# Kernel optimization log

Hardware: AMD Instinct MI355X
Metric: run time of the kernel (lower is better)

## Reference

```python
import jax, jax.numpy as jnp
import numpy as np

TOPK = 5

def _l2norm(x, axis):
    n = jnp.sqrt(jnp.sum(x * x, axis=axis, keepdims=True))
    return x / jnp.maximum(n, 1e-12)

def _conv_block(x, w, b, g, beta):
    # Conv2d(k=3, stride=2, pad=1) + BatchNorm (train-mode batch stats) + ReLU + AvgPool2d(3,1,pad=1)
    x = jax.lax.conv_general_dilated(x, w, (2, 2), ((1, 1), (1, 1)),
                                     dimension_numbers=('NCHW', 'OIHW', 'NCHW'))
    x = x + b[None, :, None, None]
    mean = jnp.mean(x, axis=(0, 2, 3), keepdims=True)
    var = jnp.mean((x - mean) ** 2, axis=(0, 2, 3), keepdims=True)
    x = (x - mean) * jax.lax.rsqrt(var + 1e-5) * g[None, :, None, None] + beta[None, :, None, None]
    x = jax.nn.relu(x)
    # AvgPool2d default count_include_pad=True -> always divide by 9
    x = jax.lax.reduce_window(x, 0.0, jax.lax.add, (1, 1, 3, 3), (1, 1, 1, 1),
                              ((0, 0), (0, 0), (1, 1), (1, 1))) / 9.0
    return x

def _encode(x, params):
    x = x[:, None]  # B,1,T,D
    for (w, b, g, beta) in params:
        x = _conv_block(x, w, b, g, beta)
    return jnp.mean(x, axis=(2, 3))  # AdaptiveAvgPool2d(1) + flatten

def setup_inputs() -> dict:
    key = jax.random.key(0)
    ks = jax.random.split(key, 8)
    B, T, D = 128, 1024, 128
    dim, capQ, refD = 128, 2048, 2304
    inp = {}
    inp['feats'] = jax.random.normal(ks[0], (B, 2, T, D), jnp.float32)
    inp['ref_feats'] = jax.random.normal(ks[1], (B, refD), jnp.float32)
    inp['indices'] = jax.random.randint(ks[2], (B,), 0, 10000)
    mq = jax.random.normal(ks[3], (dim, capQ), jnp.float32)
    inp['MoCoQueue'] = mq / jnp.maximum(jnp.linalg.norm(mq, axis=0, keepdims=True), 1e-12)
    rq = jax.random.normal(ks[4], (refD, capQ), jnp.float32)
    inp['RefQueue'] = rq / jnp.maximum(jnp.linalg.norm(rq, axis=0, keepdims=True), 1e-12)
    inp['IndexQueue'] = jax.random.randint(ks[5], (capQ,), 0, 10000).astype(jnp.float32)
    chans = [1, 4, 16, 64, 128]
    pk = jax.random.split(ks[6], 4)
    for i in range(4):
        ci, co = chans[i], chans[i + 1]
        inp['w%d' % (i + 1)] = jax.random.normal(pk[i], (co, ci, 3, 3), jnp.float32) * 0.1
        inp['b%d' % (i + 1)] = jnp.zeros((co,), jnp.float32)
        inp['g%d' % (i + 1)] = jnp.ones((co,), jnp.float32)
        inp['be%d' % (i + 1)] = jnp.zeros((co,), jnp.float32)
    return inp

def reference(feats, ref_feats, indices, MoCoQueue, RefQueue, IndexQueue,
              w1, b1, g1, be1, w2, b2, g2, be2, w3, b3, g3, be3, w4, b4, g4, be4):
    params = [(w1, b1, g1, be1), (w2, b2, g2, be2), (w3, b3, g3, be3), (w4, b4, g4, be4)]
    q = _l2norm(_encode(feats[:, 1], params), 1)                      # B,dim
    k = jax.lax.stop_gradient(_l2norm(_encode(feats[:, 0], params), 1))
    ref = _l2norm(ref_feats, 1)                                       # B,2304
    B = q.shape[0]
    score_pos = jnp.sum(q * k, axis=1, keepdims=True)                 # B,1
    score_neg = q @ jax.lax.stop_gradient(MoCoQueue)                  # B,capQ
    mask = indices[:, None].astype(IndexQueue.dtype) == IndexQueue[None, :]  # B,capQ bool
    # queue_full=True branch: topk over reference queue similarities + scatter reweighting
    score_ref = ref @ jax.lax.stop_gradient(RefQueue)                 # B,capQ
    masked = jnp.where(mask, -jnp.inf, score_ref)
    _, idx = jax.lax.top_k(masked, TOPK)                              # B,topK
    score_ref2 = jnp.where(mask, 1.0, score_ref)
    rows = jnp.arange(B)[:, None]
    weighted = jnp.full_like(score_neg, -1.0).at[rows, idx].set(1.0)
    mask_f = mask.astype(jnp.float32).at[rows, idx].set(1.0)
    score_neg = score_neg * score_ref2 * weighted
    score = jnp.concatenate([score_pos, score_neg], axis=1)           # B,1+capQ
    mask_out = jnp.concatenate([jnp.ones((B, 1), jnp.float32), mask_f], axis=1)
    return score, mask_out
```

## Files before the change

### kernel.cpp

```cpp
#include <hip/hip_runtime.h>


#define NIMG 128
typedef __attribute__((ext_vector_type(8))) short bf16x8;
typedef __attribute__((ext_vector_type(4))) float f32x4;
typedef __attribute__((ext_vector_type(4))) unsigned int u32x4;
typedef unsigned long long ull;

__device__ __forceinline__ unsigned short f2bf(float f) {
  unsigned u = __float_as_uint(f);
  unsigned r = (u + 0x7fffu + ((u >> 16) & 1u)) >> 16;
  return (unsigned short)r;
}
__device__ __forceinline__ float bf2f(unsigned short u) {
  return __uint_as_float((unsigned)u << 16);
}

__global__ __launch_bounds__(256) void wtr4_k(
    const float* __restrict__ w2, const float* __restrict__ w3,
    const float* __restrict__ w4, unsigned short* __restrict__ wb2,
    unsigned short* __restrict__ wb3, unsigned short* __restrict__ wb4) {
  const int i = blockIdx.x * 256 + threadIdx.x;
  if (i < 16 * 64) {
    int co = i / 64, k = i % 64;
    int tap = k >> 2, ci = k & 3;
    float v = (k < 36) ? w2[co * 36 + ci * 9 + tap] : 0.f;
    wb2[i] = f2bf(v);
  }
  if (i < 64 * 160) {
    int co = i / 160, k = i % 160;
    int tap = k >> 4, ci = k & 15;
    float v = (k < 144) ? w3[co * 144 + ci * 9 + tap] : 0.f;
    wb3[i] = f2bf(v);
  }
  if (i < 128 * 576) {
    int co = i / 576, k = i % 576;
    int tap = k / 64, ci = k & 63;
    wb4[i] = f2bf(w4[co * 576 + ci * 9 + tap]);
  }
}

__device__ __forceinline__ void l1row(const float* __restrict__ ib, int ih,
                                      int w0i, float* r) {
  if (ih < 0) {
#pragma unroll
    for (int q = 0; q < 9; ++q) r[q] = 0.f;
    return;
  }
  const float* rp = ib + ih * 128 + 2 * w0i;
  const float4 a = *(const float4*)rp;
  const float4 b = *(const float4*)(rp + 4);
  r[0] = (w0i > 0) ? rp[-1] : 0.f;
  r[1] = a.x; r[2] = a.y; r[3] = a.z; r[4] = a.w;
  r[5] = b.x; r[6] = b.y; r[7] = b.z; r[8] = b.w;
}

__global__ __launch_bounds__(256, 4) void conv1s_k(const float* __restrict__ feats,
    const float* __restrict__ w1, const float* __restrict__ b1,
    unsigned short* __restrict__ y, float* __restrict__ part1,
    float* __restrict__ part2) {
  constexpr int TH = 4;
  const int tid = threadIdx.x;
  const int lw = tid & 15, grp = tid >> 4;
  const int h0 = (blockIdx.x * 16 + grp) * TH;
  const int pn = blockIdx.z;
  const int p = pn >> 7, n = pn & 127;
  const int sel = (p == 0) ? 1 : 0;
  const float* ib = feats + (size_t)(n * 2 + sel) * 131072;
  const int w0i = lw * 4;

  float wgt[36];
#pragma unroll
  for (int t = 0; t < 36; ++t) wgt[t] = w1[t];
  float bv[4];
#pragma unroll
  for (int c = 0; c < 4; ++c) bv[c] = b1[c];

  float r[9][9];
#pragma unroll
  for (int j = 0; j < 9; ++j) l1row(ib, 2 * h0 - 1 + j, w0i, r[j]);

  float s1[4] = {0.f, 0.f, 0.f, 0.f}, s2[4] = {0.f, 0.f, 0.f, 0.f};
#pragma unroll
  for (int t = 0; t < TH; ++t) {
    const int h = h0 + t;
    const float* r0 = r[2 * t];
    const float* r1 = r[2 * t + 1];
    const float* r2 = r[2 * t + 2];
#pragma unroll
    for (int co = 0; co < 4; ++co) {
      unsigned short ob[4];
#pragma unroll
      for (int i = 0; i < 4; ++i) {
        float v = bv[co];
#pragma unroll
        for (int kw = 0; kw < 3; ++kw) {
          v = fmaf(wgt[co * 9 + kw],     r0[2 * i + kw], v);
          v = fmaf(wgt[co * 9 + 3 + kw], r1[2 * i + kw], v);
          v = fmaf(wgt[co * 9 + 6 + kw], r2[2 * i + kw], v);
        }
        ob[i] = f2bf(v);
        s1[co] += v; s2[co] += v * v;
      }
      const ull o = (ull)ob[0] | ((ull)ob[1] << 16) | ((ull)ob[2] << 32)
                  | ((ull)ob[3] << 48);
      *(ull*)(y + (((size_t)pn * 4 + co) * 512 + h) * 64 + w0i) = o;
    }
  }
  __shared__ float ws1[4][4], ws2[4][4];
  const int lane = tid & 63, wid = tid >> 6;
#pragma unroll
  for (int co = 0; co < 4; ++co) {
#pragma unroll
    for (int m = 32; m >= 1; m >>= 1) {
      s1[co] += __shfl_xor(s1[co], m);
      s2[co] += __shfl_xor(s2[co], m);
    }
    if (lane == 0) { ws1[wid][co] = s1[co]; ws2[wid][co] = s2[co]; }
  }
  __syncthreads();
  if (tid < 4) {
    const float t1 = ws1[0][tid] + ws1[1][tid] + ws1[2][tid] + ws1[3][tid];
    const float t2 = ws2[0][tid] + ws2[1][tid] + ws2[2][tid] + ws2[3][tid];
    const int nblk = gridDim.x * 128;
    const int blk = (pn & 127) * gridDim.x + blockIdx.x;
    part1[(size_t)(p * 4 + tid) * nblk + blk] = t1;
    part2[(size_t)(p * 4 + tid) * nblk + blk] = t2;
  }
}

template<int Cin, int H, int W, int M, int SPB, int KP, int KC, int WCO, int WSP,
         int Cout, int MSPLIT>
__global__ __launch_bounds__(256) void cgemmi_k(
    const unsigned short* __restrict__ x,
    const unsigned short* __restrict__ wb,
    const float* __restrict__ bias, unsigned short* __restrict__ y,
    float* __restrict__ part1, float* __restrict__ part2) {
  constexpr int Ho = H / 2, Wo = W / 2, HWout = Ho * Wo;
  constexpr int lgWo = (Wo == 8 ? 3 : (Wo == 16 ? 4 : 5));
  constexpr int lgCin = (Cin == 4 ? 2 : (Cin == 16 ? 4 : 6));
  constexpr int MB = M / MSPLIT;
  constexpr int KCP = KC + 8;
  constexpr int MT = WCO / 16, NT = WSP / 16, KS = KC / 32;
  constexpr int NWN = SPB / WSP;
  constexpr int GR = (Cin < 8) ? 4 : 8;
  __shared__ unsigned short wl[MB][KCP];
  __shared__ unsigned short bl[SPB][KCP];
  __shared__ float ss1[MB], ss2[MB];
  const int tid = threadIdx.x;
  const int pnl = blockIdx.y;
  const int p = pnl >> 7;
  const int spc = blockIdx.x / MSPLIT;
  const int mc = blockIdx.x - spc * MSPLIT;
  const int sp0 = spc * SPB;
  const int m0 = mc * MB;
  const int lane = tid & 63, wid = tid >> 6;
  const int wm = wid / NWN, wn = wid - wm * NWN;
  const int l15 = lane & 15, lg = lane >> 4;
  const unsigned short* xb = x + (size_t)pnl * Cin * (H * W);

  for (int i = tid; i < MB; i += 256) { ss1[i] = 0.f; ss2[i] = 0.f; }

  f32x4 acc[MT][NT];
#pragma unroll
  for (int mt = 0; mt < MT; ++mt)
#pragma unroll
    for (int nt = 0; nt < NT; ++nt) acc[mt][nt] = (f32x4){0.f, 0.f, 0.f, 0.f};

  for (int k0 = 0; k0 < KP; k0 += KC) {
    for (int it = tid; it < MB * (KC / 8); it += 256) {
      const int row = it / (KC / 8), seg = it - row * (KC / 8);
      const u32x4 v = *(const u32x4*)(wb + (size_t)(m0 + row) * KP + k0 + seg * 8);
      *(u32x4*)(&wl[row][seg * 8]) = v;
    }
    for (int it = tid; it < SPB * (KC / GR); it += 256) {
      const int row = it / (KC / GR);
      const int rem = it - row * (KC / GR);
      const int k = k0 + rem * GR;
      const int tap = k >> lgCin;
      const int ci0 = k & (Cin - 1);
      const int sp = sp0 + row;
      const int ho = sp >> lgWo, wo = sp & (Wo - 1);
      const int kh = tap / 3, kw = tap - kh * 3;
      const int ih = 2 * ho - 1 + kh, iw = 2 * wo - 1 + kw;
      unsigned short* dst = &bl[row][k - k0];
      if (tap < 9 && (unsigned)ih < (unsigned)H && (unsigned)iw < (unsigned)W) {
        const unsigned short* src = xb + ((size_t)(ih * W + iw) * Cin + ci0);
        if constexpr (GR == 4) {
          *(ull*)dst = *(const ull*)src;
        } else {
          *(u32x4*)dst = *(const u32x4*)src;
        }
      } else {
        *(ull*)dst = 0ull;
        if constexpr (GR == 8) *(ull*)(dst + 4) = 0ull;
      }
    }
    __syncthreads();
#pragma unroll
    for (int ks = 0; ks < KS; ++ks) {
      bf16x8 af[MT], bfr[NT];
#pragma unroll
      for (int mt = 0; mt < MT; ++mt)
        af[mt] = *(const bf16x8*)(&wl[wm * WCO + mt * 16 + l15][ks * 32 + lg * 8]);
#pragma unroll
      for (int nt = 0; nt < NT; ++nt)
        bfr[nt] = *(const bf16x8*)(&bl[wn * WSP + nt * 16 + l15][ks * 32 + lg * 8]);
#pragma unroll
      for (int mt = 0; mt < MT; ++mt)
#pragma unroll
        for (int nt = 0; nt < NT; ++nt)
          acc[mt][nt] = __builtin_amdgcn_mfma_f32_16x16x32_bf16(af[mt], bfr[nt], acc[mt][nt], 0, 0, 0);
    }
    __syncthreads();
  }

  unsigned short* yb = y + (size_t)pnl * Cout * HWout;
#pragma unroll
  for (int mt = 0; mt < MT; ++mt) {
#pragma unroll
    for (int i = 0; i < 4; ++i) {
      const int col = wm * WCO + mt * 16 + lg * 4 + i;
      const int co = m0 + col;
      const float bv = bias[co];
      float s1 = 0.f, s2 = 0.f;
#pragma unroll
      for (int nt = 0; nt < NT; ++nt) {
        const float v = acc[mt][nt][i] + bv;
        yb[(size_t)co * HWout + sp0 + wn * WSP + nt * 16 + l15] = f2bf(v);
        s1 += v; s2 += v * v;
      }
#pragma unroll
      for (int m = 1; m < 16; m <<= 1) { s1 += __shfl_xor(s1, m); s2 += __shfl_xor(s2, m); }
      if (l15 == 0) {
        atomicAdd(&ss1[col], s1);
        atomicAdd(&ss2[col], s2);
      }
    }
  }
  __syncthreads();
  const int nspc = gridDim.x / MSPLIT;
  const int nblk = nspc * 128;
  const int blkid = (pnl & 127) * nspc + spc;
  for (int i = tid; i < MB; i += 256) {
    part1[(size_t)(p * Cout + m0 + i) * nblk + blkid] = ss1[i];
    part2[(size_t)(p * Cout + m0 + i) * nblk + blkid] = ss2[i];
  }
}

__global__ __launch_bounds__(256) void redstat_k(const float* __restrict__ p1,
    const float* __restrict__ p2, float* __restrict__ st, int nblk) {
  const int row = blockIdx.x;
  float s1 = 0.f, s2 = 0.f;
  for (int i = threadIdx.x; i < nblk; i += 256) {
    s1 += p1[(size_t)row * nblk + i];
    s2 += p2[(size_t)row * nblk + i];
  }
  __shared__ float r1[256], r2[256];
  r1[threadIdx.x] = s1; r2[threadIdx.x] = s2;
  __syncthreads();
  for (int stp = 128; stp > 0; stp >>= 1) {
    if (threadIdx.x < stp) {
      r1[threadIdx.x] += r1[threadIdx.x + stp];
      r2[threadIdx.x] += r2[threadIdx.x + stp];
    }
    __syncthreads();
  }
  if (threadIdx.x == 0) {
    st[row] = r1[0];
    st[256 + row] = r2[0];
  }
}

template<int W>
__device__ __forceinline__ void row_hs(const unsigned short* __restrict__ yp,
                                       int hh, int H, int w0, float a, float b,
                                       float* hs) {
  if ((unsigned)hh >= (unsigned)H) { hs[0] = hs[1] = hs[2] = hs[3] = 0.f; return; }
  const unsigned short* rp = yp + hh * W;
  const ull B = *(const ull*)(rp + w0);
  float r0 = 0.f, r5 = 0.f;
  if (w0 > 0) r0 = fmaxf(fmaf(a, bf2f(rp[w0 - 1]), b), 0.f);
  if (w0 + 4 < W) r5 = fmaxf(fmaf(a, bf2f(rp[w0 + 4]), b), 0.f);
  const float r1 = fmaxf(fmaf(a, bf2f((unsigned short)(B & 0xffff)), b), 0.f);
  const float r2 = fmaxf(fmaf(a, bf2f((unsigned short)((B >> 16) & 0xffff)), b), 0.f);
  const float r3 = fmaxf(fmaf(a, bf2f((unsigned short)((B >> 32) & 0xffff)), b), 0.f);
  const float r4 = fmaxf(fmaf(a, bf2f((unsigned short)(B >> 48)), b), 0.f);
  hs[0] = r0 + r1 + r2;
  hs[1] = r1 + r2 + r3;
  hs[2] = r2 + r3 + r4;
  hs[3] = r3 + r4 + r5;
}

template<int Cout, int H, int W>
__global__ __launch_bounds__(256) void bnpool7_k(const unsigned short* __restrict__ y,
    const float* __restrict__ st, const float* __restrict__ g,
    const float* __restrict__ be, unsigned short* __restrict__ x4, float invCnt) {
  constexpr int W4 = W / 4;
  constexpr int lgW4 = (W4 == 16 ? 4 : (W4 == 8 ? 3 : 2));
  constexpr int NCG = Cout / 4;
  constexpr int lgNCG = (NCG == 1 ? 0 : (NCG == 4 ? 2 : 4));
  constexpr int HQ = 256 >> (lgW4 + lgNCG);
  constexpr int TH = 4;
  constexpr int R = HQ * TH;
  constexpr int RS = W * Cout;
  constexpr int RSP = RS + 8;
  constexpr int HW = H * W;
  __shared__ unsigned short lbuf[R * RSP];
  const int tid = threadIdx.x;
  const int wq = tid & (W4 - 1);
  const int cg = (tid >> lgW4) & (NCG - 1);
  const int hq = tid >> (lgW4 + lgNCG);
  const int w0 = wq * 4;
  const int c0 = cg * 4;
  const int h0 = blockIdx.x * R;
  const int ht0 = h0 + hq * TH;
  const int pn = blockIdx.z;
  const int p = pn >> 7;

  float a[4], b[4];
#pragma unroll
  for (int j = 0; j < 4; ++j) {
    const int c = c0 + j;
    const float mean = st[p * Cout + c] * invCnt;
    const float var = fmaxf(st[256 + p * Cout + c] * invCnt - mean * mean, 0.f);
    a[j] = g[c] * rsqrtf(var + 1e-5f);
    b[j] = be[c] - mean * a[j];
  }
  const unsigned short* yb = y + (size_t)pn * Cout * (size_t)HW;

  float hsA[4][4], hsB[4][4], hsC[4][4];
#pragma unroll
  for (int j = 0; j < 4; ++j)
    row_hs<W>(yb + (size_t)(c0 + j) * HW, ht0 - 1, H, w0, a[j], b[j], hsA[j]);
#pragma unroll
  for (int j = 0; j < 4; ++j)
    row_hs<W>(yb + (size_t)(c0 + j) * HW, ht0, H, w0, a[j], b[j], hsB[j]);
#pragma unroll
  for (int t = 0; t < TH; ++t) {
    const int h = ht0 + t;
    const int lh = hq * TH + t;
#pragma unroll
    for (int j = 0; j < 4; ++j)
      row_hs<W>(yb + (size_t)(c0 + j) * HW, h + 1, H, w0, a[j], b[j], hsC[j]);
#pragma unroll
    for (int i = 0; i < 4; ++i) {
      unsigned short ob[4];
#pragma unroll
      for (int j = 0; j < 4; ++j)
        ob[j] = f2bf((hsA[j][i] + hsB[j][i] + hsC[j][i]) * (1.f / 9.f));
      const ull o = (ull)ob[0] | ((ull)ob[1] << 16) | ((ull)ob[2] << 32)
                  | ((ull)ob[3] << 48);
      *(ull*)(&lbuf[lh * RSP + (w0 + i) * Cout + c0]) = o;
    }
#pragma unroll
    for (int j = 0; j < 4; ++j)
#pragma unroll
      for (int i = 0; i < 4; ++i) { hsA[j][i] = hsB[j][i]; hsB[j][i] = hsC[j][i]; }
  }
  __syncthreads();
  unsigned short* xp = x4 + ((size_t)pn * HW + (size_t)h0 * W) * Cout;
  constexpr int SEGS = RS / 8;
  for (int it = tid; it < R * SEGS; it += 256) {
    const int row = it / SEGS, seg = it - row * SEGS;
    const u32x4 v = *(const u32x4*)(&lbuf[row * RSP + seg * 8]);
    *(u32x4*)(xp + (size_t)row * RS + seg * 8) = v;
  }
}

template<int Cout, int H, int W, int TH>
__global__ __launch_bounds__(256) void bnpool3_k(const unsigned short* __restrict__ y,
    const float* __restrict__ st, const float* __restrict__ g,
    const float* __restrict__ be, unsigned short* __restrict__ x, float invCnt) {
  constexpr int W4 = W / 4;
  constexpr int GROUPS = 256 / W4;
  constexpr int HW = H * W;
  const int tid = threadIdx.x;
  const int grp = tid / W4, lw = tid - grp * W4;
  const int w0 = lw * 4;
  const int h0 = (blockIdx.x * GROUPS + grp) * TH;
  if (h0 >= H) return;
  const int pn = blockIdx.z, c = blockIdx.y;
  const int p = pn >> 7;
  const float mean = st[p * Cout + c] * invCnt;
  const float var = fmaxf(st[256 + p * Cout + c] * invCnt - mean * mean, 0.f);
  const float a = g[c] * rsqrtf(var + 1e-5f);
  const float b = be[c] - mean * a;
  const unsigned short* yp = y + ((size_t)pn * Cout + c) * (size_t)HW;
  unsigned short* xp = x + ((size_t)pn * Cout + c) * (size_t)HW;

  float hsA[4], hsB[4], hsC[4];
  row_hs<W>(yp, h0 - 1, H, w0, a, b, hsA);
  row_hs<W>(yp, h0, H, w0, a, b, hsB);
#pragma unroll
  for (int t = 0; t < TH; ++t) {
    const int h = h0 + t;
    if (h >= H) break;
    row_hs<W>(yp, h + 1, H, w0, a, b, hsC);
    const ull o = (ull)f2bf((hsA[0] + hsB[0] + hsC[0]) * (1.f / 9.f))
                | ((ull)f2bf((hsA[1] + hsB[1] + hsC[1]) * (1.f / 9.f)) << 16)
                | ((ull)f2bf((hsA[2] + hsB[2] + hsC[2]) * (1.f / 9.f)) << 32)
                | ((ull)f2bf((hsA[3] + hsB[3] + hsC[3]) * (1.f / 9.f)) << 48);
    *(ull*)(xp + h * W + w0) = o;
#pragma unroll
    for (int i = 0; i < 4; ++i) { hsA[i] = hsB[i]; hsB[i] = hsC[i]; }
  }
}

__global__ __launch_bounds__(256) void feat2_k(const unsigned short* __restrict__ x,
    float* __restrict__ qk, float* __restrict__ qkT) {
  const int pn = blockIdx.x;
  const int tid = threadIdx.x;
  const int lane = tid & 63, wid = tid >> 6;
  __shared__ float fm[128];
  __shared__ float red[128];
  const unsigned short* xb = x + (size_t)pn * 128 * 512;
  for (int c = wid; c < 128; c += 4) {
    const unsigned short* xp = xb + (size_t)c * 512;
    float s = 0.f;
#pragma unroll
    for (int r = 0; r < 4; ++r) {
      const unsigned v = *(const unsigned*)(xp + lane * 2 + r * 128);
      s += bf2f((unsigned short)(v & 0xffff)) + bf2f((unsigned short)(v >> 16));
    }
#pragma unroll
    for (int m = 32; m >= 1; m >>= 1) s += __shfl_xor(s, m);
    if (lane == 0) fm[c] = s * (1.f / 512.f);
  }
  __syncthreads();
  if (tid < 128) red[tid] = fm[tid] * fm[tid];
  __syncthreads();
  for (int step = 64; step > 0; step >>= 1) {
    if (tid < step) red[tid] += red[tid + step];
    __syncthreads();
  }
  const float inv = 1.f / fmaxf(sqrtf(red[0]), 1e-12f);
  if (tid < 128) {
    const float v = fm[tid] * inv;
    qk[(size_t)pn * 128 + tid] = v;
    if (pn < 128) qkT[(size_t)tid * 128 + pn] = v;
  }
}

__global__ __launch_bounds__(256) void refnorm_k(const float* __restrict__ rf,
    float* __restrict__ rinv) {
  const int n = blockIdx.x;
  float s = 0.f;
  for (int i = threadIdx.x; i < 2304; i += 256) {
    float v = rf[(size_t)n * 2304 + i];
    s += v * v;
  }
  __shared__ float red[256];
  red[threadIdx.x] = s;
  __syncthreads();
  for (int step = 128; step > 0; step >>= 1) {
    if (threadIdx.x < step) red[threadIdx.x] += red[threadIdx.x + step];
    __syncthreads();
  }
  if (threadIdx.x == 0) rinv[n] = 1.f / fmaxf(sqrtf(red[0]), 1e-12f);
}

__global__ __launch_bounds__(256) void reft_k(const float* __restrict__ rf,
    const float* __restrict__ rinv, float* __restrict__ rfT) {
  const int flat = blockIdx.x * 256 + threadIdx.x;
  const int n = flat / 2304, k = flat - n * 2304;
  rfT[(size_t)k * 128 + n] = rf[flat] * rinv[n];
}

__global__ __launch_bounds__(256) void sneg2_k(const float* __restrict__ qkT,
    const float* __restrict__ moco, float* __restrict__ out) {
  const int j = blockIdx.x * 256 + threadIdx.x;
  const int n0 = blockIdx.y * 8;
  float acc[8] = {0.f};
#pragma unroll 4
  for (int k = 0; k < 128; ++k) {
    const float rv = moco[(size_t)k * 2048 + j];
    const float* qp = qkT + (size_t)k * 128 + n0;
#pragma unroll
    for (int i = 0; i < 8; ++i) acc[i] = fmaf(qp[i], rv, acc[i]);
  }
#pragma unroll
  for (int i = 0; i < 8; ++i) out[(size_t)(n0 + i) * 2048 + j] = acc[i];
}

template<int KCH>
__global__ __launch_bounds__(256) void sref3_k(const float* __restrict__ rfT,
    const float* __restrict__ rq, float* __restrict__ part) {
  const int j = blockIdx.x * 256 + threadIdx.x;
  const int n0 = blockIdx.y * 8;
  const int kc = blockIdx.z;
  const int kbeg = kc * KCH;
  float acc[8] = {0.f};
#pragma unroll 4
  for (int k = kbeg; k < kbeg + KCH; ++k) {
    const float rv = rq[(size_t)k * 2048 + j];
    const float* rp = rfT + (size_t)k * 128 + n0;
#pragma unroll
    for (int i = 0; i < 8; ++i) acc[i] = fmaf(rp[i], rv, acc[i]);
  }
  float* pb = part + (size_t)kc * (128 * 2048);
#pragma unroll
  for (int i = 0; i < 8; ++i) pb[(size_t)(n0 + i) * 2048 + j] = acc[i];
}

template<int NCH>
__global__ __launch_bounds__(256) void sredr_k(const float* __restrict__ part,
    float* __restrict__ out) {
  const int j = blockIdx.x * 256 + threadIdx.x;
  const int n = blockIdx.y;
  const size_t off = (size_t)n * 2048 + j;
  float s = 0.f;
#pragma unroll
  for (int c = 0; c < NCH; ++c) s += part[(size_t)c * (128 * 2048) + off];
  out[off] = s;
}

__global__ __launch_bounds__(256) void topk_k(const float* __restrict__ sref,
    const float* __restrict__ iq, const int* __restrict__ idxs,
    int* __restrict__ top) {
  const int n = blockIdx.x;
  const float target = (float)idxs[n];
  float vals[8];
#pragma unroll
  for (int r = 0; r < 8; ++r) {
    const int j = threadIdx.x + r * 256;
    const bool m = (iq[j] == target);
    vals[r] = m ? -__builtin_inff() : sref[(size_t)n * 2048 + j];
  }
  __shared__ float sv[256];
  __shared__ int si[256];
  __shared__ int chosen[5];
  for (int rnd = 0; rnd < 5; ++rnd) {
    float bv = -__builtin_inff();
    int bi = 1 << 30;
#pragma unroll
    for (int r = 0; r < 8; ++r) {
      const int j = threadIdx.x + r * 256;
      bool taken = false;
      for (int t = 0; t < rnd; ++t) taken |= (chosen[t] == j);
      const float v = vals[r];
      if (!taken && (v > bv || (v == bv && j < bi))) { bv = v; bi = j; }
    }
    sv[threadIdx.x] = bv; si[threadIdx.x] = bi;
    __syncthreads();
    for (int step = 128; step > 0; step >>= 1) {
      if (threadIdx.x < step) {
        const float ov = sv[threadIdx.x + step];
        const int oi = si[threadIdx.x + step];
        if (ov > sv[threadIdx.x] || (ov == sv[threadIdx.x] && oi < si[threadIdx.x])) {
          sv[threadIdx.x] = ov; si[threadIdx.x] = oi;
        }
      }
      __syncthreads();
    }
    if (threadIdx.x == 0) chosen[rnd] = si[0];
    __syncthreads();
  }
  if (threadIdx.x < 5) top[n * 5 + threadIdx.x] = chosen[threadIdx.x];
}

__global__ __launch_bounds__(128) void spos_k(const float* __restrict__ qk,
    float* __restrict__ out) {
  const int n = threadIdx.x;
  float s = 0.f;
  for (int c = 0; c < 128; ++c)
    s = fmaf(qk[(size_t)n * 128 + c], qk[(size_t)(NIMG + n) * 128 + c], s);
  out[(size_t)n * 2049] = s;
  out[(size_t)NIMG * 2049 + (size_t)n * 2049] = 1.f;
}

__global__ __launch_bounds__(256) void asm_k(const float* __restrict__ sneg,
    const float* __restrict__ sref, const float* __restrict__ iq,
    const int* __restrict__ idxs, const int* __restrict__ top,
    float* __restrict__ out) {
  const int n = blockIdx.y;
  const int j = blockIdx.x * 256 + threadIdx.x;
  const int t0 = top[n * 5 + 0], t1 = top[n * 5 + 1], t2 = top[n * 5 + 2];
  const int t3 = top[n * 5 + 3], t4 = top[n * 5 + 4];
  const float target = (float)idxs[n];
  const bool m = (iq[j] == target);
  const float sr = sref[(size_t)n * 2048 + j];
  const float sr2 = m ? 1.f : sr;
  const bool istop = (j == t0) | (j == t1) | (j == t2) | (j == t3) | (j == t4);
  const float wgt = istop ? 1.f : -1.f;
  out[(size_t)n * 2049 + 1 + j] = sneg[(size_t)n * 2048 + j] * sr2 * wgt;
  const float mf = istop ? 1.f : (m ? 1.f : 0.f);
  out[(size_t)NIMG * 2049 + (size_t)n * 2049 + 1 + j] = mf;
}

extern "C" void kernel_launch(void* const* d_in, const int* in_sizes, int n_in,
                              void* d_out, int out_size, void* d_ws, size_t ws_size,
                              hipStream_t stream) {
  const float* feats = (const float*)d_in[0];
  const float* reff  = (const float*)d_in[1];
  const int*   idxs  = (const int*)d_in[2];
  const float* moco  = (const float*)d_in[3];
  const float* refq  = (const float*)d_in[4];
  const float* iq    = (const float*)d_in[5];
  const float* w[4]  = {(const float*)d_in[6],  (const float*)d_in[10],
                        (const float*)d_in[14], (const float*)d_in[18]};
  const float* b[4]  = {(const float*)d_in[7],  (const float*)d_in[11],
                        (const float*)d_in[15], (const float*)d_in[19]};
  const float* g[4]  = {(const float*)d_in[8],  (const float*)d_in[12],
                        (const float*)d_in[16], (const float*)d_in[20]};
  const float* be[4] = {(const float*)d_in[9],  (const float*)d_in[13],
                        (const float*)d_in[17], (const float*)d_in[21]};
  float* out = (float*)d_out;

  const size_t BIG = 33554432;
  unsigned short* X = (unsigned short*)d_ws;
  unsigned short* Y = X + BIG;
  float* ST   = (float*)(Y + BIG);
  unsigned short* WB2 = (unsigned short*)(ST + 2048);
  unsigned short* WB3 = WB2 + 1024;
  unsigned short* WB4 = WB3 + 10240;
  float* QK   = (float*)(WB4 + 73728);
  float* QKT  = QK + 32768;
  float* RINV = QKT + 16384;
  float* RFT  = RINV + 128;
  float* SNEG = RFT + 294912;
  float* SREF = SNEG + 262144;
  int*   TOP  = (int*)(SREF + 262144);
  float* SPART = (float*)(TOP + 256);
  unsigned short* X4 = (unsigned short*)(SPART + 6 * 128 * 2048);
  float* PART1 = SNEG;
  float* PART2 = SNEG + 131072;

  wtr4_k<<<288, 256, 0, stream>>>(w[1], w[2], w[3], WB2, WB3, WB4);

  conv1s_k<<<dim3(8, 1, 256), 256, 0, stream>>>(feats, w[0], b[0], Y, PART1, PART2);
  redstat_k<<<8, 256, 0, stream>>>(PART1, PART2, ST, 1024);
  bnpool7_k<4, 512, 64><<<dim3(8, 1, 256), 256, 0, stream>>>(Y, ST, g[0], be[0], X4,
                                                             1.f / (128.f * 32768.f));
  cgemmi_k<4, 512, 64, 16, 256, 64, 64, 16, 64, 16, 1>
      <<<dim3(32, 256), 256, 0, stream>>>(X4, WB2, b[1], Y, PART1, PART2);
  redstat_k<<<32, 256, 0, stream>>>(PART1, PART2, ST + 512, 32 * 128);
  bnpool7_k<16, 256, 32><<<dim3(8, 1, 256), 256, 0, stream>>>(Y, ST + 512, g[1], be[1], X4,
                                                              1.f / (128.f * 8192.f));
  cgemmi_k<16, 256, 32, 64, 256, 160, 32, 64, 64, 64, 1>
      <<<dim3(8, 256), 256, 0, stream>>>(X4, WB3, b[2], Y, PART1, PART2);
  redstat_k<<<128, 256, 0, stream>>>(PART1, PART2, ST + 1024, 8 * 128);
  bnpool7_k<64, 128, 16><<<dim3(8, 1, 256), 256, 0, stream>>>(Y, ST + 1024, g[2], be[2], X4,
                                                              1.f / (128.f * 2048.f));
  cgemmi_k<64, 128, 16, 128, 128, 576, 64, 32, 64, 128, 2>
      <<<dim3(8, 256), 256, 0, stream>>>(X4, WB4, b[3], Y, PART1, PART2);
  redstat_k<<<256, 256, 0, stream>>>(PART1, PART2, ST + 1536, 4 * 128);
  bnpool3_k<128, 64, 8, 1><<<dim3(1, 128, 256), 256, 0, stream>>>(Y, ST + 1536, g[3], be[3], X,
                                                                  1.f / (128.f * 512.f));

  feat2_k<<<256, 256, 0, stream>>>(X, QK, QKT);
  refnorm_k<<<128, 256, 0, stream>>>(reff, RINV);
  reft_k<<<1152, 256, 0, stream>>>(reff, RINV, RFT);
  sneg2_k<<<dim3(8, 16), 256, 0, stream>>>(QKT, moco, SNEG);
  sref3_k<384><<<dim3(8, 16, 6), 256, 0, stream>>>(RFT, refq, SPART);
  sredr_k<6><<<dim3(8, 128), 256, 0, stream>>>(SPART, SREF);
  topk_k<<<128, 256, 0, stream>>>(SREF, iq, idxs, TOP);
  spos_k<<<1, 128, 0, stream>>>(QK, out);
  asm_k<<<dim3(8, 128), 256, 0, stream>>>(SNEG, SREF, iq, idxs, TOP, out);
}
```

Measured before the change: 579.0 us.

## Load implicit-GEMM conv operands directly from global into MFMA registers, drop LDS staging

The implicit-GEMM convolution kernel no longer stages weight and im2col tiles through shared memory with barriers. Each lane now computes its own im2col addresses and loads bf16x8 fragments straight from global memory into MFMA operands, with zero-fill for padding and out-of-range taps. Per-variant occupancy hints are added through launch bounds. This removes LDS traffic and syncthreads, but each wave now reloads overlapping input and weight data from global memory and cache, with no reuse across waves.

```diff
diff --git a/kernel.cpp b/kernel.cpp
--- a/kernel.cpp
+++ b/kernel.cpp
@@ -129,9 +129,15 @@
   }
 }
 
-template<int Cin, int H, int W, int M, int SPB, int KP, int KC, int WCO, int WSP,
-         int Cout, int MSPLIT>
-__global__ __launch_bounds__(256) void cgemmi_k(
+__device__ __forceinline__ bf16x8 ld16z(const unsigned short* p, bool ok) {
+  u32x4 v = *(const u32x4*)p;
+  if (!ok) v = (u32x4){0u, 0u, 0u, 0u};
+  union { u32x4 a; bf16x8 b; } u; u.a = v; return u.b;
+}
+
+template<int Cin, int H, int W, int M, int SPB, int KP, int WCO, int WSP,
+         int Cout, int MSPLIT, int WAVES>
+__global__ __launch_bounds__(256, WAVES) void cgemmr_k(
     const unsigned short* __restrict__ x,
     const unsigned short* __restrict__ wb,
     const float* __restrict__ bias, unsigned short* __restrict__ y,
@@ -140,12 +146,8 @@
   constexpr int lgWo = (Wo == 8 ? 3 : (Wo == 16 ? 4 : 5));
   constexpr int lgCin = (Cin == 4 ? 2 : (Cin == 16 ? 4 : 6));
   constexpr int MB = M / MSPLIT;
-  constexpr int KCP = KC + 8;
-  constexpr int MT = WCO / 16, NT = WSP / 16, KS = KC / 32;
+  constexpr int MT = WCO / 16, NT = WSP / 16, KS = KP / 32;
   constexpr int NWN = SPB / WSP;
-  constexpr int GR = (Cin < 8) ? 4 : 8;
-  __shared__ unsigned short wl[MB][KCP];
-  __shared__ unsigned short bl[SPB][KCP];
   __shared__ float ss1[MB], ss2[MB];
   const int tid = threadIdx.x;
   const int pnl = blockIdx.y;
@@ -160,6 +162,15 @@
   const unsigned short* xb = x + (size_t)pnl * Cin * (H * W);
 
   for (int i = tid; i < MB; i += 256) { ss1[i] = 0.f; ss2[i] = 0.f; }
+  __syncthreads();
+
+  int ihb[NT], iwb[NT];
+#pragma unroll
+  for (int nt = 0; nt < NT; ++nt) {
+    const int sp = sp0 + wn * WSP + nt * 16 + l15;
+    ihb[nt] = 2 * (sp >> lgWo) - 1;
+    iwb[nt] = 2 * (sp & (Wo - 1)) - 1;
+  }
 
   f32x4 acc[MT][NT];
 #pragma unroll
@@ -167,52 +178,49 @@
 #pragma unroll
     for (int nt = 0; nt < NT; ++nt) acc[mt][nt] = (f32x4){0.f, 0.f, 0.f, 0.f};
 
-  for (int k0 = 0; k0 < KP; k0 += KC) {
-    for (int it = tid; it < MB * (KC / 8); it += 256) {
-      const int row = it / (KC / 8), seg = it - row * (KC / 8);
-      const u32x4 v = *(const u32x4*)(wb + (size_t)(m0 + row) * KP + k0 + seg * 8);
-      *(u32x4*)(&wl[row][seg * 8]) = v;
-    }
-    for (int it = tid; it < SPB * (KC / GR); it += 256) {
-      const int row = it / (KC / GR);
-      const int rem = it - row * (KC / GR);
-      const int k = k0 + rem * GR;
-      const int tap = k >> lgCin;
-      const int ci0 = k & (Cin - 1);
-      const int sp = sp0 + row;
-      const int ho = sp >> lgWo, wo = sp & (Wo - 1);
-      const int kh = tap / 3, kw = tap - kh * 3;
-      const int ih = 2 * ho - 1 + kh, iw = 2 * wo - 1 + kw;
-      unsigned short* dst = &bl[row][k - k0];
-      if (tap < 9 && (unsigned)ih < (unsigned)H && (unsigned)iw < (unsigned)W) {
-        const unsigned short* src = xb + ((size_t)(ih * W + iw) * Cin + ci0);
-        if constexpr (GR == 4) {
-          *(ull*)dst = *(const ull*)src;
-        } else {
-          *(u32x4*)dst = *(const u32x4*)src;
+#pragma unroll
+  for (int ks = 0; ks < KS; ++ks) {
+    const int kbase = ks * 32 + lg * 8;
+    bf16x8 af[MT];
+#pragma unroll
+    for (int mt = 0; mt < MT; ++mt)
+      af[mt] = *(const bf16x8*)(wb + (size_t)(m0 + wm * WCO + mt * 16 + l15) * KP
+                                + kbase);
+    bf16x8 bfr[NT];
+#pragma unroll
+    for (int nt = 0; nt < NT; ++nt) {
+      if constexpr (Cin >= 8) {
+        const int tap = kbase >> lgCin;
+        const int ci0 = kbase & (Cin - 1);
+        const int kh = tap / 3, kw = tap - kh * 3;
+        const int ih = ihb[nt] + kh, iw = iwb[nt] + kw;
+        const bool ok = (tap < 9) & ((unsigned)ih < (unsigned)H)
+                      & ((unsigned)iw < (unsigned)W);
+        const int off = ok ? ((ih * W + iw) * Cin + ci0) : 0;
+        bfr[nt] = ld16z(xb + off, ok);
+      } else {
+        ull hv[2];
+#pragma unroll
+        for (int hh = 0; hh < 2; ++hh) {
+          const int tap = (kbase >> 2) + hh;
+          const int kh = tap / 3, kw = tap - kh * 3;
+          const int ih = ihb[nt] + kh, iw = iwb[nt] + kw;
+          const bool ok = (tap < 9) & ((unsigned)ih < (unsigned)H)
+                        & ((unsigned)iw < (unsigned)W);
+          const int off = ok ? ((ih * W + iw) * 4) : 0;
+          const ull v = *(const ull*)(xb + off);
+          hv[hh] = ok ? v : 0ull;
         }
-      } else {
-        *(ull*)dst = 0ull;
-        if constexpr (GR == 8) *(ull*)(dst + 4) = 0ull;
+        union { ull u[2]; bf16x8 b; } uu;
+        uu.u[0] = hv[0]; uu.u[1] = hv[1];
+        bfr[nt] = uu.b;
       }
     }
-    __syncthreads();
-#pragma unroll
-    for (int ks = 0; ks < KS; ++ks) {
-      bf16x8 af[MT], bfr[NT];
-#pragma unroll
-      for (int mt = 0; mt < MT; ++mt)
-        af[mt] = *(const bf16x8*)(&wl[wm * WCO + mt * 16 + l15][ks * 32 + lg * 8]);
+#pragma unroll
+    for (int mt = 0; mt < MT; ++mt)
 #pragma unroll
       for (int nt = 0; nt < NT; ++nt)
-        bfr[nt] = *(const bf16x8*)(&bl[wn * WSP + nt * 16 + l15][ks * 32 + lg * 8]);
-#pragma unroll
-      for (int mt = 0; mt < MT; ++mt)
-#pragma unroll
-        for (int nt = 0; nt < NT; ++nt)
-          acc[mt][nt] = __builtin_amdgcn_mfma_f32_16x16x32_bf16(af[mt], bfr[nt], acc[mt][nt], 0, 0, 0);
-    }
-    __syncthreads();
+        acc[mt][nt] = __builtin_amdgcn_mfma_f32_16x16x32_bf16(af[mt], bfr[nt], acc[mt][nt], 0, 0, 0);
   }
 
   unsigned short* yb = y + (size_t)pnl * Cout * HWout;
@@ -632,17 +640,17 @@
   redstat_k<<<8, 256, 0, stream>>>(PART1, PART2, ST, 1024);
   bnpool7_k<4, 512, 64><<<dim3(8, 1, 256), 256, 0, stream>>>(Y, ST, g[0], be[0], X4,
                                                              1.f / (128.f * 32768.f));
-  cgemmi_k<4, 512, 64, 16, 256, 64, 64, 16, 64, 16, 1>
+  cgemmr_k<4, 512, 64, 16, 256, 64, 16, 64, 16, 1, 6>
       <<<dim3(32, 256), 256, 0, stream>>>(X4, WB2, b[1], Y, PART1, PART2);
   redstat_k<<<32, 256, 0, stream>>>(PART1, PART2, ST + 512, 32 * 128);
   bnpool7_k<16, 256, 32><<<dim3(8, 1, 256), 256, 0, stream>>>(Y, ST + 512, g[1], be[1], X4,
                                                               1.f / (128.f * 8192.f));
-  cgemmi_k<16, 256, 32, 64, 256, 160, 32, 64, 64, 64, 1>
+  cgemmr_k<16, 256, 32, 64, 256, 160, 64, 64, 64, 1, 3>
       <<<dim3(8, 256), 256, 0, stream>>>(X4, WB3, b[2], Y, PART1, PART2);
   redstat_k<<<128, 256, 0, stream>>>(PART1, PART2, ST + 1024, 8 * 128);
   bnpool7_k<64, 128, 16><<<dim3(8, 1, 256), 256, 0, stream>>>(Y, ST + 1024, g[2], be[2], X4,
                                                               1.f / (128.f * 2048.f));
-  cgemmi_k<64, 128, 16, 128, 128, 576, 64, 32, 64, 128, 2>
+  cgemmr_k<64, 128, 16, 128, 128, 576, 32, 64, 128, 2, 4>
       <<<dim3(8, 256), 256, 0, stream>>>(X4, WB4, b[3], Y, PART1, PART2);
   redstat_k<<<256, 256, 0, stream>>>(PART1, PART2, ST + 1536, 4 * 128);
   bnpool3_k<128, 64, 8, 1><<<dim3(1, 128, 256), 256, 0, stream>>>(Y, ST + 1536, g[3], be[3], X,
```

After: 581.0 us. No clear change (+0.3%).
